# Kernel optimization log

Hardware: AMD Instinct MI355X
Metric: run time of the kernel (lower is better)

Reference implementation:

```python
import jax, jax.numpy as jnp
import numpy as np

K = 8  # leader_num
S = 8  # state_num


def setup_inputs() -> dict:
    key = jax.random.key(0)
    ks = jax.random.split(key, 11)
    B, L, C, H = 16, 720, 128, 96
    F2 = H // 2 + 1
    OUT = F2 * (2 * K + 1)
    return {
        "x": jax.random.normal(ks[0], (B, L, C), jnp.float32),
        "y_hat": jax.random.normal(ks[1], (B, H, C), jnp.float32),
        "temperature": jnp.ones((1,), jnp.float32),
        "cls_w": jax.random.normal(ks[2], (S, L), jnp.float32) * 0.02,
        "basic_state": jax.random.normal(ks[3], (C, S), jnp.float32) * 0.02,
        "state_bias": jax.random.normal(ks[4], (S,), jnp.float32) * 0.02,
        "mix_head_w": jax.random.normal(ks[5], (S, K * OUT), jnp.float32) * 0.05,
        "mix_head_b": jax.random.normal(ks[6], (S, OUT), jnp.float32) * 0.05,
        "mix_wr": jax.random.normal(ks[7], (F2, 3 * F2), jnp.float32) * 0.05,
        "mix_wi": jax.random.normal(ks[8], (F2, 3 * F2), jnp.float32) * 0.05,
        "mix_br": jax.random.normal(ks[9], (F2,), jnp.float32) * 0.05,
        "mix_bi": jax.random.normal(ks[10], (F2,), jnp.float32) * 0.05,
    }


def _leader_pipeline(xn, yn):
    # xn: [B,C,L] instance-normed lookback, yn: [B,C,H] normed forecast
    B, C, L = xn.shape
    H = yn.shape[-1]
    rf = jnp.fft.rfft(xn, axis=-1)  # [B,C,F]
    # full pairwise circular cross-correlation: [B,C,C,L]
    cc = jnp.fft.irfft(rf[:, :, None, :] * jnp.conj(rf)[:, None, :, :], n=L, axis=-1)
    ca = jnp.abs(cc)
    # local-max masking on interior points (drops first/last lag)
    mask = (ca[..., 1:-1] >= ca[..., :-2]) & (ca[..., 1:-1] >= ca[..., 2:])
    cc = cc[..., 1:-1] * mask / L  # [B,C,C,L-2]
    ca = jnp.abs(cc)
    shift = jnp.argmax(ca, axis=-1)  # [B,C,C] best lag per pair
    cmax = jnp.max(ca, axis=-1)
    _, leader_ids = jax.lax.top_k(cmax, K)  # [B,C,K]
    lead_corr = jnp.take_along_axis(cc, leader_ids[:, :, :, None], axis=2)  # [B,C,K,L-2]
    shift = jnp.take_along_axis(shift, leader_ids, axis=2)  # [B,C,K]
    r = jnp.take_along_axis(lead_corr, shift[..., None], axis=3)[..., 0]  # [B,C,K]
    shift = shift + 1  # account for the dropped first lag (local_max=True)
    # gather leader sequences and apply per-(sample,channel,leader) dynamic shift
    const_idx = jnp.arange(L, L + H)
    idx = const_idx[None, None, :] - shift.reshape(B, C * K, 1)  # [B,CK,H]
    seq = jnp.concatenate([xn, yn], -1)  # [B,C,L+H]
    seq = seq[jnp.arange(B)[:, None], leader_ids.reshape(B, C * K)]  # [B,CK,L+H]
    seq_shifted = jnp.take_along_axis(seq, idx, axis=-1).reshape(B, C, K, H)
    seq_shifted = seq_shifted * jnp.sign(r)[..., None]
    return seq_shifted, jnp.abs(r)


def reference(x, y_hat, temperature, cls_w, basic_state, state_bias,
              mix_head_w, mix_head_b, mix_wr, mix_wi, mix_br, mix_bi):
    B, L, C = x.shape
    H = y_hat.shape[1]
    F2 = H // 2 + 1
    xt = jnp.swapaxes(x, 1, 2)  # [B,C,L]
    yt = jnp.swapaxes(y_hat, 1, 2)  # [B,C,H]
    mu = xt.mean(-1, keepdims=True)
    xc = xt - mu
    std = jnp.sqrt((xc ** 2).mean(-1, keepdims=True) + 1e-8)
    xn = xc / std
    yn = (yt - mu) / std
    seq_shifted, r_abs = _leader_pipeline(xn, yn)  # torch.no_grad block
    seq_shifted = jax.lax.stop_gradient(seq_shifted)
    r_abs = jax.lax.stop_gradient(r_abs)
    ones = jnp.ones((B, C, 1), xt.dtype)
    rw = jax.nn.softmax(jnp.concatenate([ones, r_abs], -1) / temperature, axis=-1)
    corr_feat = rw[..., 1:]  # [B,C,K]
    # FilterFactory (num_state > 1, need_classifier): per-sample state mixture
    p = jax.nn.softmax(state_bias + basic_state + jnp.einsum('bcl,sl->bcs', xt, cls_w), axis=-1)  # [B,C,S]
    OUT = F2 * (2 * K + 1)
    w = jnp.einsum('bcs,sf->bcf', p, mix_head_w).reshape(B, C, K, OUT)
    b = jnp.einsum('bcs,so->bco', p, mix_head_b)
    filt = (jnp.einsum('bck,bcko->bco', corr_feat, w) + b).reshape(B, C, 2 * K + 1, F2)
    yf = jnp.fft.rfft(yn, axis=-1)  # [B,C,F2] complex64
    ssf = jnp.fft.rfft(seq_shifted, axis=-1) * filt[:, :, :K]  # [B,C,K,F2]
    sdf = (ssf - yf[:, :, None]) * filt[:, :, K:2 * K]
    yff = yf * filt[:, :, -1]
    catf = jnp.concatenate([ssf.sum(2), sdf.sum(2), yff], -1)  # [B,C,3*F2]
    mix_w = jax.lax.complex(mix_wr, mix_wi)  # [F2, 3*F2]
    mix_b = jax.lax.complex(mix_br, mix_bi)
    out_f = jnp.einsum('bcf,of->bco', catf, mix_w) + mix_b
    yn_new = yn + jnp.fft.irfft(out_f, n=H, axis=-1)
    y = yn_new * std + mu
    return jnp.swapaxes(y, 1, 2)  # [B,H,C]
```

## Files before the change

### kernel.cpp

```cpp
#include <hip/hip_runtime.h>
#include <math.h>

#define B_ 16
#define L_ 720
#define C_ 128
#define H_ 96
#define F2_ 49
#define K_ 8
#define S_ 8
#define OUT_ 833
#define SEQLEN 816
#define NF 361

__device__ __forceinline__ float2 cmulp(float2 a, float2 w) {
  return make_float2(a.x*w.x - a.y*w.y, a.x*w.y + a.y*w.x);
}

#define WSYNC() do { asm volatile("s_waitcnt lgkmcnt(0)" ::: "memory"); __builtin_amdgcn_sched_barrier(0); } while (0)

__device__ __constant__ float W5X[5] = {1.f, 0.30901699437494742f, -0.80901699437494745f, -0.80901699437494745f, 0.30901699437494742f};
__device__ __constant__ float W5Y[5] = {0.f, 0.95105651629515357f, 0.58778525229247312f, -0.58778525229247312f, -0.95105651629515357f};

__device__ __forceinline__ void dft8_pos(const float2 zin[8], float2 X[8]) {
  const float RH = 0.70710678118654752440f;
  const float2 A0 = make_float2(zin[0].x+zin[4].x, zin[0].y+zin[4].y);
  const float2 A1 = make_float2(zin[0].x-zin[4].x, zin[0].y-zin[4].y);
  const float2 A2 = make_float2(zin[2].x+zin[6].x, zin[2].y+zin[6].y);
  const float2 A3 = make_float2(zin[2].x-zin[6].x, zin[2].y-zin[6].y);
  const float2 A4 = make_float2(zin[1].x+zin[5].x, zin[1].y+zin[5].y);
  const float2 A5 = make_float2(zin[1].x-zin[5].x, zin[1].y-zin[5].y);
  const float2 A6 = make_float2(zin[3].x+zin[7].x, zin[3].y+zin[7].y);
  const float2 A7 = make_float2(zin[3].x-zin[7].x, zin[3].y-zin[7].y);
  const float2 B0 = make_float2(A0.x+A2.x, A0.y+A2.y);
  const float2 B1 = make_float2(A0.x-A2.x, A0.y-A2.y);
  const float2 B2 = make_float2(A4.x+A6.x, A4.y+A6.y);
  const float2 B3 = make_float2(A4.x-A6.x, A4.y-A6.y);
  X[0] = make_float2(B0.x+B2.x, B0.y+B2.y);
  X[4] = make_float2(B0.x-B2.x, B0.y-B2.y);
  X[2] = make_float2(B1.x - B3.y, B1.y + B3.x);
  X[6] = make_float2(B1.x + B3.y, B1.y - B3.x);
  const float2 CI   = make_float2(-A3.y, A3.x);
  const float2 W1s1 = make_float2((A5.x - A5.y)*RH, (A5.x + A5.y)*RH);
  const float2 W3s1 = make_float2((-A5.x - A5.y)*RH, (A5.x - A5.y)*RH);
  const float2 W1s3 = make_float2((A7.x - A7.y)*RH, (A7.x + A7.y)*RH);
  const float2 W3s3 = make_float2((-A7.x - A7.y)*RH, (A7.x - A7.y)*RH);
  X[1] = make_float2(A1.x + CI.x + W1s1.x + W3s3.x, A1.y + CI.y + W1s1.y + W3s3.y);
  X[5] = make_float2(A1.x + CI.x - W1s1.x - W3s3.x, A1.y + CI.y - W1s1.y - W3s3.y);
  X[3] = make_float2(A1.x - CI.x + W3s1.x + W1s3.x, A1.y - CI.y + W3s1.y + W1s3.y);
  X[7] = make_float2(A1.x - CI.x - W3s1.x - W1s3.x, A1.y - CI.y - W3s1.y - W1s3.y);
}

__global__ __launch_bounds__(256) void k0_tab(float2* __restrict__ wtab_g) {
  for (int k = threadIdx.x; k < L_; k += 256) {
    double ang = (double)k * 0.008726646259971647884;
    wtab_g[k] = make_float2((float)cos(ang), (float)sin(ang));
  }
}

__global__ __launch_bounds__(256) void k1_fused(const float* __restrict__ x,
                                                const float* __restrict__ yh,
                                                const float2* __restrict__ wtab_g,
                                                float* __restrict__ seq,
                                                float* __restrict__ mu_g,
                                                float* __restrict__ std_g,
                                                float2* __restrict__ Rc) {
  const int bc0 = blockIdx.x * 2;
  const int b = bc0 >> 7, c0 = bc0 & 127;
  const int tid = threadIdx.x;
  __shared__ float xrow[2][L_];
  __shared__ float yrow[2][H_];
  __shared__ float2 wt[L_];
  __shared__ float red[4];

  const float* xb = x + (size_t)b * L_ * C_ + c0;
  for (int l = tid; l < L_; l += 256) {
    const float2 v = *(const float2*)&xb[(size_t)l * C_];
    xrow[0][l] = v.x; xrow[1][l] = v.y;
  }
  const float* yb = yh + (size_t)b * H_ * C_ + c0;
  if (tid < H_) {
    const float2 v = *(const float2*)&yb[(size_t)tid * C_];
    yrow[0][tid] = v.x; yrow[1][tid] = v.y;
  }
  for (int k = tid; k < L_; k += 256) wt[k] = wtab_g[k];
  __syncthreads();

  for (int ch = 0; ch < 2; ++ch) {
    float s = 0.f;
    for (int l = tid; l < L_; l += 256) s += xrow[ch][l];
    for (int off = 32; off; off >>= 1) s += __shfl_down(s, off, 64);
    if ((tid & 63) == 0) red[tid >> 6] = s;
    __syncthreads();
    const float mu = (red[0] + red[1] + red[2] + red[3]) * (1.0f / L_);
    __syncthreads();
    float vs = 0.f;
    for (int l = tid; l < L_; l += 256) { float d = xrow[ch][l] - mu; vs += d * d; }
    for (int off = 32; off; off >>= 1) vs += __shfl_down(vs, off, 64);
    if ((tid & 63) == 0) red[tid >> 6] = vs;
    __syncthreads();
    const float stdv = sqrtf((red[0] + red[1] + red[2] + red[3]) * (1.0f / L_) + 1e-8f);
    const float inv = 1.0f / stdv;
    if (tid == 0) { mu_g[bc0 + ch] = mu; std_g[bc0 + ch] = stdv; }
    __syncthreads();
    float* sq = seq + (size_t)(bc0 + ch) * SEQLEN;
    for (int l = tid; l < L_; l += 256) { const float v = (xrow[ch][l] - mu) * inv; xrow[ch][l] = v; sq[l] = v; }
    if (tid < H_) sq[L_ + tid] = (yrow[ch][tid] - mu) * inv;
    __syncthreads();
  }

  for (int u = tid; u < 2 * NF; u += 256) {
    const int row = u / NF, f = u - row * NF;
    float re = 0.f, im = 0.f;
    int m = 0;
    const float* xr = xrow[row];
    for (int l = 0; l < L_; ++l) {
      const float v = xr[l];
      const float2 w = wt[m];
      re = fmaf(v, w.x, re);
      im = fmaf(-v, w.y, im);
      m += f; if (m >= L_) m -= L_;
    }
    Rc[(size_t)(bc0 + row) * NF + f] = make_float2(re, im);
  }
}

__global__ __launch_bounds__(256, 3) void k2_fft(const float2* __restrict__ Rc,
                                                 const float2* __restrict__ wtab_g,
                                                 float* __restrict__ r_arr,
                                                 int* __restrict__ t_arr) {
  const int phys = blockIdx.x;
  int idx = (phys & 7) * 1152 + (phys >> 3);
  const int b = idx / 576;
  idx -= b * 576;
  int g = 0;
  while (true) { const int cnt = (8 - g) << 4; if (idx < cnt) break; idx -= cnt; ++g; }
  const int rows = 8 - g;
  const int c1 = (g << 4) + idx / rows;
  const int c2t = g + idx % rows;
  const int c2base = c2t << 4;
  const int tid = threadIdx.x;
  const int wid = tid >> 6, lane = tid & 63;

  __shared__ float2 r1c[NF];
  __shared__ float2 t9[81];
  __shared__ float2 t45[45];
  __shared__ float2 Yw[4][360];
  __shared__ __align__(16) float ccw[4][728];

  for (int f = tid; f < NF; f += 256) r1c[f] = Rc[((size_t)(b * C_ + c1)) * NF + f];
  for (int i = tid; i < 81; i += 256) { int a = i / 9, c = i % 9; t9[i] = wtab_g[80 * ((a * c) % 9)]; }
  for (int i = tid; i < 45; i += 256) { int bb = i / 9, c = i % 9; t45[i] = wtab_g[16 * bb * c]; }
  __syncthreads();

  const float SCALE = 1.0f / 518400.0f;

  for (int j = 0; j < 4; ++j) {
    const int c2 = c2base + (wid << 2) + j;
    if (c2 < c1) continue;
    const float2* R2 = Rc + ((size_t)(b * C_ + c2)) * NF;

    for (int k = lane; k < 360; k += 64) {
      const int fB = 360 - k;
      const float2 a1 = r1c[k];
      const float2 a2 = r1c[fB];
      const float2 b1 = R2[k];
      const float2 b2 = R2[fB];
      const float2 pA = make_float2(a1.x*b1.x + a1.y*b1.y, a1.y*b1.x - a1.x*b1.y);
      float2 pB = make_float2(a2.x*b2.x + a2.y*b2.y, a2.y*b2.x - a2.x*b2.y);
      pB.y = (k == 0) ? pB.y : -pB.y;
      const float2 E = make_float2(pA.x + pB.x, pA.y + pB.y);
      const float2 O = make_float2(pA.x - pB.x, pA.y - pB.y);
      const float2 Ow = cmulp(O, wtab_g[k]);
      Yw[wid][k] = make_float2(E.x - Ow.y, E.y + Ow.x);
    }
    WSYNC();

    if (lane < 45) {
      const int K2 = lane;
      float2 zin[8];
#pragma unroll
      for (int q1 = 0; q1 < 8; ++q1) zin[q1] = Yw[wid][45 * q1 + K2];
      float2 X[8];
      dft8_pos(zin, X);
      int m = 0;
#pragma unroll
      for (int n1 = 0; n1 < 8; ++n1) {
        Yw[wid][n1 * 45 + K2] = cmulp(X[n1], wtab_g[m]);
        m += 2 * K2;
      }
    }
    WSYNC();

    {
      auto s2_task = [&](int t) {
        const int n1 = t / 9;
        const int c  = t - 9 * n1;
        const float2* Yrow = &Yw[wid][n1 * 45];
        float yr[5], yi[5];
#pragma unroll
        for (int d = 0; d < 5; ++d) { yr[d] = 0.f; yi[d] = 0.f; }
#pragma unroll 1
        for (int bq = 0; bq < 5; ++bq) {
          float ur = 0.f, ui = 0.f;
#pragma unroll
          for (int a = 0; a < 9; ++a) {
            const float2 zv = Yrow[5 * a + bq];
            const float2 tv = t9[9 * a + c];
            ur += zv.x * tv.x - zv.y * tv.y;
            ui += zv.x * tv.y + zv.y * tv.x;
          }
          const float2 tw = t45[9 * bq + c];
          const float vr = ur * tw.x - ui * tw.y;
          const float vi = ur * tw.y + ui * tw.x;
#pragma unroll
          for (int d = 0; d < 5; ++d) {
            const int m = (bq * d) % 5;
            yr[d] += vr * W5X[m] - vi * W5Y[m];
            yi[d] += vr * W5Y[m] + vi * W5X[m];
          }
        }
        float2* cc2 = (float2*)(&ccw[wid][0]);
#pragma unroll
        for (int d = 0; d < 5; ++d)
          cc2[n1 + 8 * (c + 9 * d)] = make_float2(yr[d], yi[d]);
      };
      s2_task(lane);
      __builtin_amdgcn_sched_barrier(0);
      if (lane < 8) s2_task(64 + lane);
      __builtin_amdgcn_sched_barrier(0);
    }
    WSYNC();

    {
      const float* cr = ccw[wid];
      float bvF = 0.f; int btF = 1;
      float bvM = 0.f; int uM  = 719;
      for (int i = lane; i < 719; i += 64) {
        const int u = i + 1;
        const float v  = fabsf(cr[u]);
        const float lf = fabsf(cr[u - 1]);
        const float rt = fabsf(cr[(u == 719) ? 0 : (u + 1)]);
        if (v >= lf && v >= rt) {
          if (u <= 718 && (v > bvF || (v == bvF && u < btF))) { bvF = v; btF = u; }
          if (u >= 2   && (v > bvM || (v == bvM && u > uM)))  { bvM = v; uM  = u; }
        }
      }
      for (int off = 32; off; off >>= 1) {
        const float ovF = __shfl_down(bvF, off, 64); const int otF = __shfl_down(btF, off, 64);
        if (ovF > bvF || (ovF == bvF && otF < btF)) { bvF = ovF; btF = otF; }
        const float ovM = __shfl_down(bvM, off, 64); const int ouM = __shfl_down(uM, off, 64);
        if (ovM > bvM || (ovM == bvM && ouM > uM)) { bvM = ovM; uM = ouM; }
      }
      if (lane == 0) {
        const float rF = (bvF > 0.f) ? cr[btF] * SCALE : 0.f;
        const size_t o = ((size_t)(b * C_ + c1)) * C_ + c2;
        r_arr[o] = rF; t_arr[o] = btF;
        if (c2 > c1) {
          const float rM = (bvM > 0.f) ? cr[uM] * SCALE : 0.f;
          const size_t o2 = ((size_t)(b * C_ + c2)) * C_ + c1;
          r_arr[o2] = rM; t_arr[o2] = 720 - uM;
        }
      }
    }
    WSYNC();
  }
}

__global__ __launch_bounds__(256) void k34_fused(const float* __restrict__ x,
                                                 const float* __restrict__ temperature,
                                                 const float* __restrict__ cls_w,
                                                 const float* __restrict__ basic_state,
                                                 const float* __restrict__ state_bias,
                                                 const float* __restrict__ mhw,
                                                 const float* __restrict__ mhb,
                                                 const float* __restrict__ r_arr,
                                                 const int* __restrict__ t_arr,
                                                 const float* __restrict__ seq,
                                                 const float* __restrict__ mu_g,
                                                 const float* __restrict__ std_g,
                                                 const float* __restrict__ mwr,
                                                 const float* __restrict__ mwi,
                                                 const float* __restrict__ mbr,
                                                 const float* __restrict__ mbi,
                                                 float* __restrict__ out) {
  const int bc = blockIdx.x;
  const int b = bc >> 7, c = bc & 127;
  const int tid = threadIdx.x;
  __shared__ float caL[C_], rL[C_];
  __shared__ int tL[C_];
  __shared__ float xrowL[L_];
  __shared__ float cfL[K_], srL[K_], pL[S_], qL[S_ * K_], praw[S_];
  __shared__ int leadL[K_], ltL[K_];
  __shared__ float cosT[96], sinT[96];
  __shared__ float ssL[K_][H_], ynL[H_], flL[OUT_];
  __shared__ float sfr[K_][F2_], sfi[K_][F2_], yfr[F2_], yfi[F2_];
  __shared__ float catr[3 * F2_], cati[3 * F2_], ofr[F2_], ofi[F2_];

  const float* xb = x + (size_t)b * L_ * C_ + c;
  for (int l = tid; l < L_; l += 256) xrowL[l] = xb[(size_t)l * C_];
  if (tid < C_) {
    const float r = r_arr[(size_t)bc * C_ + tid];
    rL[tid] = r; caL[tid] = fabsf(r);
    tL[tid] = t_arr[(size_t)bc * C_ + tid];
  }
  if (tid >= 128 && tid < 224) {
    const int h = tid - 128;
    const float ang = (float)h * (float)(6.283185307179586 / 96.0);
    cosT[h] = cosf(ang); sinT[h] = sinf(ang);
    ynL[h] = seq[(size_t)bc * SEQLEN + L_ + h];
  }
  __syncthreads();

  if (tid == 0) {
    const float T = temperature[0];
    float lg[K_ + 1];
    lg[0] = 1.0f / T;
    for (int k = 0; k < K_; ++k) {
      float bvv = -1.f; int bi = 0;
      for (int jj = 0; jj < C_; ++jj) { const float v = caL[jj]; if (v > bvv) { bvv = v; bi = jj; } }
      leadL[k] = bi; ltL[k] = tL[bi];
      const float rv = rL[bi];
      srL[k] = (rv > 0.f) ? 1.f : ((rv < 0.f) ? -1.f : 0.f);
      lg[k + 1] = bvv / T;
      caL[bi] = -2.f;
    }
    float m = lg[0];
    for (int k = 1; k <= K_; ++k) m = fmaxf(m, lg[k]);
    float sum = 0.f, e[K_ + 1];
    for (int k = 0; k <= K_; ++k) { e[k] = expf(lg[k] - m); sum += e[k]; }
    const float invs = 1.0f / sum;
    for (int k = 0; k < K_; ++k) cfL[k] = e[k + 1] * invs;
  }

  {
    const int gg = tid >> 5, lane = tid & 31;
    float acc = 0.f;
    const float* w = cls_w + (size_t)gg * L_;
    for (int l = lane; l < L_; l += 32) acc += xrowL[l] * w[l];
    for (int off = 16; off; off >>= 1) acc += __shfl_down(acc, off, 32);
    if (lane == 0) praw[gg] = acc + state_bias[gg] + basic_state[c * S_ + gg];
  }
  __syncthreads();
  if (tid == 0) {
    float m = praw[0];
    for (int s2 = 1; s2 < S_; ++s2) m = fmaxf(m, praw[s2]);
    float sum = 0.f;
    for (int s2 = 0; s2 < S_; ++s2) { const float e = expf(praw[s2] - m); pL[s2] = e; sum += e; }
    const float invs = 1.0f / sum;
    for (int s2 = 0; s2 < S_; ++s2) pL[s2] *= invs;
    for (int s2 = 0; s2 < S_; ++s2)
      for (int k = 0; k < K_; ++k) qL[s2 * K_ + k] = pL[s2] * cfL[k];
  }
  __syncthreads();

  for (int o = tid; o < OUT_; o += 256) {
    float acc = 0.f;
#pragma unroll
    for (int s2 = 0; s2 < S_; ++s2) {
      acc += pL[s2] * mhb[s2 * OUT_ + o];
#pragma unroll
      for (int k = 0; k < K_; ++k)
        acc += qL[s2 * K_ + k] * mhw[(size_t)s2 * (K_ * OUT_) + k * OUT_ + o];
    }
    flL[o] = acc;
  }
  for (int i = tid; i < K_ * H_; i += 256) {
    const int k = i / H_, h = i - k * H_;
    ssL[k][h] = seq[((size_t)(b * C_ + leadL[k])) * SEQLEN + (L_ + h - ltL[k])] * srL[k];
  }
  __syncthreads();

  for (int u = tid; u < K_ * F2_ + F2_; u += 256) {
    if (u < K_ * F2_) {
      const int k = u / F2_, f = u - k * F2_;
      float re = 0.f, im = 0.f; int m = 0;
      for (int h = 0; h < H_; ++h) {
        const float v = ssL[k][h];
        re = fmaf(v, cosT[m], re); im = fmaf(-v, sinT[m], im);
        m += f; if (m >= 96) m -= 96;
      }
      sfr[k][f] = re; sfi[k][f] = im;
    } else {
      const int f = u - K_ * F2_;
      float re = 0.f, im = 0.f; int m = 0;
      for (int h = 0; h < H_; ++h) {
        const float v = ynL[h];
        re = fmaf(v, cosT[m], re); im = fmaf(-v, sinT[m], im);
        m += f; if (m >= 96) m -= 96;
      }
      yfr[f] = re; yfi[f] = im;
    }
  }
  __syncthreads();

  if (tid < F2_) {
    const int f = tid;
    float s1r = 0.f, s1i = 0.f, s2r = 0.f, s2i = 0.f;
    const float yr = yfr[f], yi = yfi[f];
#pragma unroll
    for (int k = 0; k < K_; ++k) {
      const float fa = flL[k * F2_ + f], fb = flL[(K_ + k) * F2_ + f];
      const float ar = sfr[k][f] * fa, ai = sfi[k][f] * fa;
      s1r += ar; s1i += ai;
      s2r += (ar - yr) * fb; s2i += (ai - yi) * fb;
    }
    const float fc = flL[2 * K_ * F2_ + f];
    catr[f] = s1r;            cati[f] = s1i;
    catr[F2_ + f] = s2r;      cati[F2_ + f] = s2i;
    catr[2 * F2_ + f] = yr * fc; cati[2 * F2_ + f] = yi * fc;
  }
  __syncthreads();

  if (tid < F2_) {
    const int o = tid;
    float ar = mbr[o], ai = mbi[o];
    const float* wr = mwr + (size_t)o * (3 * F2_);
    const float* wi = mwi + (size_t)o * (3 * F2_);
    for (int f = 0; f < 3 * F2_; ++f) {
      const float cr = catr[f], ci = cati[f];
      const float wrr = wr[f], wii = wi[f];
      ar += cr * wrr - ci * wii;
      ai += cr * wii + ci * wrr;
    }
    ofr[o] = ar; ofi[o] = ai;
  }
  __syncthreads();

  if (tid < H_) {
    const int h = tid;
    float val = ofr[0] + ofr[48] * ((h & 1) ? -1.f : 1.f);
    int m = h;
    for (int f = 1; f < 48; ++f) {
      val += 2.f * (ofr[f] * cosT[m] - ofi[f] * sinT[m]);
      m += h; if (m >= 96) m -= 96;
    }
    val *= (1.0f / 96.0f);
    const float mu = mu_g[bc], stdv = std_g[bc];
    out[((size_t)b * H_ + h) * C_ + c] = (ynL[h] + val) * stdv + mu;
  }
}

extern "C" void kernel_launch(void* const* d_in, const int* in_sizes, int n_in,
                              void* d_out, int out_size, void* d_ws, size_t ws_size,
                              hipStream_t stream) {
  const float* x    = (const float*)d_in[0];
  const float* yh   = (const float*)d_in[1];
  const float* temp = (const float*)d_in[2];
  const float* clsw = (const float*)d_in[3];
  const float* bst  = (const float*)d_in[4];
  const float* sbias= (const float*)d_in[5];
  const float* mhw  = (const float*)d_in[6];
  const float* mhb  = (const float*)d_in[7];
  const float* mwr  = (const float*)d_in[8];
  const float* mwi  = (const float*)d_in[9];
  const float* mbr  = (const float*)d_in[10];
  const float* mbi  = (const float*)d_in[11];
  float* out = (float*)d_out;

  float* ws = (float*)d_ws;
  float* seq    = ws;
  float* mu_g   = seq + (size_t)2048 * SEQLEN;
  float* std_g  = mu_g + 2048;
  float* r_arr  = std_g + 2048;
  int*   t_arr  = (int*)(r_arr + (size_t)2048 * C_);
  float2* Rc    = (float2*)(t_arr + (size_t)2048 * C_);
  float2* wtab  = Rc + (size_t)2048 * NF;

  hipLaunchKernelGGL(k0_tab, dim3(1), dim3(256), 0, stream, wtab);
  hipLaunchKernelGGL(k1_fused, dim3(B_ * C_ / 2), dim3(256), 0, stream, x, yh, wtab, seq, mu_g, std_g, Rc);
  hipLaunchKernelGGL(k2_fft, dim3(B_ * 576), dim3(256), 0, stream, Rc, wtab, r_arr, t_arr);
  hipLaunchKernelGGL(k34_fused, dim3(B_ * C_), dim3(256), 0, stream,
                     x, temp, clsw, bst, sbias, mhw, mhb, r_arr, t_arr,
                     seq, mu_g, std_g, mwr, mwi, mbr, mbi, out);
}
```

Before: 855.8 us.

## Replace naive per-bin DFT in k1 with mixed-radix 16x45 FFT packing two channels

The first kernel used to compute the 361-bin rfft of each normalized row as a direct O(L^2) DFT loop. It now packs the two channel rows into one complex sequence and runs a 720-point FFT: a radix-16 pass with twiddles, then a 45-point stage split into 9x5 DFTs using shared-memory twiddle tables. The two real spectra are recovered from the conjugate-symmetric combination. The launch bound occupancy hint for k2 also rises from 3 to 4, which may limit registers there. Extra shared memory is used for the staging buffers, and only a subset of threads is active in each FFT stage.

```diff
diff --git a/kernel.cpp b/kernel.cpp
--- a/kernel.cpp
+++ b/kernel.cpp
@@ -18,6 +18,8 @@
 
 #define WSYNC() do { asm volatile("s_waitcnt lgkmcnt(0)" ::: "memory"); __builtin_amdgcn_sched_barrier(0); } while (0)
 
+__device__ __constant__ float W16X[10] = {1.f, 0.9238795325112867f, 0.7071067811865476f, 0.3826834323650898f, 0.f, 0.f, -0.7071067811865476f, 0.f, 0.f, -0.9238795325112867f};
+__device__ __constant__ float W16Y[10] = {0.f, 0.3826834323650898f, 0.7071067811865476f, 0.9238795325112867f, 1.f, 0.f, 0.7071067811865476f, 0.f, 0.f, -0.3826834323650898f};
 __device__ __constant__ float W5X[5] = {1.f, 0.30901699437494742f, -0.80901699437494745f, -0.80901699437494745f, 0.30901699437494742f};
 __device__ __constant__ float W5Y[5] = {0.f, 0.95105651629515357f, 0.58778525229247312f, -0.58778525229247312f, -0.95105651629515357f};
 
@@ -70,6 +72,10 @@
   __shared__ float xrow[2][L_];
   __shared__ float yrow[2][H_];
   __shared__ float2 wt[L_];
+  __shared__ float2 t9s[81];
+  __shared__ float2 t45s[45];
+  __shared__ float2 Yst[720];
+  __shared__ float2 Zp[720];
   __shared__ float red[4];
 
   const float* xb = x + (size_t)b * L_ * C_ + c0;
@@ -83,6 +89,8 @@
     yrow[0][tid] = v.x; yrow[1][tid] = v.y;
   }
   for (int k = tid; k < L_; k += 256) wt[k] = wtab_g[k];
+  for (int i = tid; i < 81; i += 256) { int a = i / 9, c = i % 9; t9s[i] = wtab_g[80 * ((a * c) % 9)]; }
+  for (int i = tid; i < 45; i += 256) { int bb = i / 9, c = i % 9; t45s[i] = wtab_g[16 * bb * c]; }
   __syncthreads();
 
   for (int ch = 0; ch < 2; ++ch) {
@@ -108,23 +116,98 @@
     __syncthreads();
   }
 
-  for (int u = tid; u < 2 * NF; u += 256) {
-    const int row = u / NF, f = u - row * NF;
-    float re = 0.f, im = 0.f;
+  if (tid < 45) {
+    const int n2 = tid;
+    float2 z[16];
+#pragma unroll
+    for (int n1 = 0; n1 < 16; ++n1) {
+      const int n = 45 * n1 + n2;
+      z[n1] = make_float2(xrow[0][n], -xrow[1][n]);
+    }
+    float2 u4[4][4];
+#pragma unroll
+    for (int bb = 0; bb < 4; ++bb) {
+      const float2 p0 = z[bb], p1 = z[4 + bb], p2 = z[8 + bb], p3 = z[12 + bb];
+      const float t0r = p0.x + p2.x, t0i = p0.y + p2.y;
+      const float t1r = p0.x - p2.x, t1i = p0.y - p2.y;
+      const float t2r = p1.x + p3.x, t2i = p1.y + p3.y;
+      const float t3r = p1.x - p3.x, t3i = p1.y - p3.y;
+      u4[bb][0] = make_float2(t0r + t2r, t0i + t2i);
+      u4[bb][2] = make_float2(t0r - t2r, t0i - t2i);
+      u4[bb][1] = make_float2(t1r - t3i, t1i + t3r);
+      u4[bb][3] = make_float2(t1r + t3i, t1i - t3r);
+    }
+#pragma unroll
+    for (int bb = 1; bb < 4; ++bb)
+#pragma unroll
+      for (int c = 1; c < 4; ++c) {
+        const float2 w = make_float2(W16X[bb * c], W16Y[bb * c]);
+        u4[bb][c] = cmulp(u4[bb][c], w);
+      }
+    float2 g16[16];
+#pragma unroll
+    for (int c = 0; c < 4; ++c) {
+      const float2 p0 = u4[0][c], p1 = u4[1][c], p2 = u4[2][c], p3 = u4[3][c];
+      const float t0r = p0.x + p2.x, t0i = p0.y + p2.y;
+      const float t1r = p0.x - p2.x, t1i = p0.y - p2.y;
+      const float t2r = p1.x + p3.x, t2i = p1.y + p3.y;
+      const float t3r = p1.x - p3.x, t3i = p1.y - p3.y;
+      g16[c + 0]  = make_float2(t0r + t2r, t0i + t2i);
+      g16[c + 8]  = make_float2(t0r - t2r, t0i - t2i);
+      g16[c + 4]  = make_float2(t1r - t3i, t1i + t3r);
+      g16[c + 12] = make_float2(t1r + t3i, t1i - t3r);
+    }
     int m = 0;
-    const float* xr = xrow[row];
-    for (int l = 0; l < L_; ++l) {
-      const float v = xr[l];
-      const float2 w = wt[m];
-      re = fmaf(v, w.x, re);
-      im = fmaf(-v, w.y, im);
-      m += f; if (m >= L_) m -= L_;
-    }
-    Rc[(size_t)(bc0 + row) * NF + f] = make_float2(re, im);
-  }
-}
-
-__global__ __launch_bounds__(256, 3) void k2_fft(const float2* __restrict__ Rc,
+#pragma unroll
+    for (int k1 = 0; k1 < 16; ++k1) {
+      Yst[k1 * 45 + n2] = cmulp(g16[k1], wt[m]);
+      m += n2;
+    }
+  }
+  __syncthreads();
+
+  if (tid < 144) {
+    const int row = tid / 9;
+    const int c = tid - 9 * row;
+    const float2* Yrow = &Yst[row * 45];
+    float yr[5], yi[5];
+#pragma unroll
+    for (int d = 0; d < 5; ++d) { yr[d] = 0.f; yi[d] = 0.f; }
+#pragma unroll 1
+    for (int bq = 0; bq < 5; ++bq) {
+      float ur = 0.f, ui = 0.f;
+#pragma unroll
+      for (int a = 0; a < 9; ++a) {
+        const float2 zv = Yrow[5 * a + bq];
+        const float2 tv = t9s[9 * a + c];
+        ur += zv.x * tv.x - zv.y * tv.y;
+        ui += zv.x * tv.y + zv.y * tv.x;
+      }
+      const float2 tw = t45s[9 * bq + c];
+      const float vr = ur * tw.x - ui * tw.y;
+      const float vi = ur * tw.y + ui * tw.x;
+#pragma unroll
+      for (int d = 0; d < 5; ++d) {
+        const int m = (bq * d) % 5;
+        yr[d] += vr * W5X[m] - vi * W5Y[m];
+        yi[d] += vr * W5Y[m] + vi * W5X[m];
+      }
+    }
+#pragma unroll
+    for (int d = 0; d < 5; ++d)
+      Zp[row + 16 * (c + 9 * d)] = make_float2(yr[d], yi[d]);
+  }
+  __syncthreads();
+
+  for (int f = tid; f < NF; f += 256) {
+    const float2 zf = Zp[f];
+    const float2 zm = Zp[(720 - f) % 720];
+    Rc[(size_t)bc0 * NF + f]       = make_float2((zf.x + zm.x) * 0.5f, (zm.y - zf.y) * 0.5f);
+    Rc[(size_t)(bc0 + 1) * NF + f] = make_float2((-zf.y - zm.y) * 0.5f, (zm.x - zf.x) * 0.5f);
+  }
+}
+
+__global__ __launch_bounds__(256, 4) void k2_fft(const float2* __restrict__ Rc,
                                                  const float2* __restrict__ wtab_g,
                                                  float* __restrict__ r_arr,
                                                  int* __restrict__ t_arr) {
```

After: 740.8 us (median of 2 runs). -13.4%, faster.
